# Kernel optimization log

Hardware: AMD Instinct MI355X
Metric: run time of the kernel (lower is better)

The kernel has to match this reference:

```python
import jax, jax.numpy as jnp
import numpy as np

B, T, NEMBD, HEAD = 8, 2048, 1024, 64

def setup_inputs() -> dict:
    key = jax.random.key(0)
    ks = jax.random.split(key, 6)
    return {
        "values": jax.random.normal(ks[0], (B, T, NEMBD), dtype=jnp.float32),
        "keys": jax.random.normal(ks[1], (B, T, NEMBD), dtype=jnp.float32),
        "queries": jax.random.normal(ks[2], (B, T, NEMBD), dtype=jnp.float32),
        "Wk": jax.random.normal(ks[3], (NEMBD, HEAD), dtype=jnp.float32) * (NEMBD ** -0.5),
        "Wq": jax.random.normal(ks[4], (NEMBD, HEAD), dtype=jnp.float32) * (NEMBD ** -0.5),
        "Wv": jax.random.normal(ks[5], (NEMBD, HEAD), dtype=jnp.float32) * (NEMBD ** -0.5),
    }

def reference(values, keys, queries, Wk, Wq, Wv):
    Bq, Tq, C = queries.shape  # C = nEmbd; original scales by C**-0.5 (NOT headSize)
    k = keys @ Wk              # [B,T,H]
    q = queries @ Wq           # [B,T,H]
    v = values @ Wv            # [B,T,H]
    weight = jnp.einsum('bth,bsh->bts', q, k) * (C ** -0.5)  # [B,T,T]
    causal = jnp.tril(jnp.ones((Tq, Tq), dtype=bool))
    weight = jnp.where(causal, weight, -jnp.inf)
    weight = jax.nn.softmax(weight, axis=-1)
    # dropout = 0.0 (eval): identity
    out = jnp.einsum('bts,bsh->bth', weight, v)  # [B,T,H]
    return out
```

## Files before the change

### kernel.cpp

```cpp
#include <hip/hip_runtime.h>
#include <hip/hip_bf16.h>

typedef __bf16 bf16x8 __attribute__((ext_vector_type(8)));
typedef float f32x4 __attribute__((ext_vector_type(4)));
typedef unsigned short u16x8 __attribute__((ext_vector_type(8)));

#define NB 8
#define NT 2048
#define NC 1024
#define NH 64

__device__ __forceinline__ unsigned short bfbits(float f) {
    return __builtin_bit_cast(unsigned short, (__bf16)f);
}

__global__ __launch_bounds__(256) void wt_kernel(const float* __restrict__ Wq,
                                                 const float* __restrict__ Wk,
                                                 const float* __restrict__ Wv,
                                                 unsigned short* __restrict__ Wt) {
    int idx = blockIdx.x * 256 + threadIdx.x;
    int n = idx >> 16;
    int r = idx & 65535;
    int c = r >> 6;
    int h = r & 63;
    const float* W = (n == 0) ? Wq : ((n == 1) ? Wk : Wv);
    float x = W[c * 64 + h];
    Wt[(n << 16) + h * 1024 + c] = bfbits(x);
}

__global__ __launch_bounds__(256, 4) void proj_kernel(const float* __restrict__ Xv,
                                                      const float* __restrict__ Xk,
                                                      const float* __restrict__ Xq,
                                                      const unsigned short* __restrict__ Wt,
                                                      unsigned short* __restrict__ Q,
                                                      unsigned short* __restrict__ K,
                                                      unsigned short* __restrict__ VT) {
    __shared__ __align__(16) char Xs[64 * 256];
    __shared__ __align__(16) char Ws[64 * 256];

    int type = blockIdx.x >> 8;
    int mt   = blockIdx.x & 255;
    int row0 = mt << 6;
    const float* X = (type == 0) ? Xq : ((type == 1) ? Xk : Xv);
    const unsigned short* W = Wt + (type << 16);

    int tid  = threadIdx.x;
    int w    = tid >> 6;
    int lane = tid & 63;
    int lo = lane & 15, hi = lane >> 4;

    f32x4 acc[4];
#pragma unroll
    for (int ct = 0; ct < 4; ++ct) acc[ct] = 0.f;

    for (int kc = 0; kc < 8; ++kc) {
        f32x4 xr[8];
#pragma unroll
        for (int i = 0; i < 8; ++i) {
            int f4 = tid + 256 * i;
            int r  = f4 >> 5, c4 = f4 & 31;
            xr[i] = __builtin_nontemporal_load(
                (const f32x4*)(X + (size_t)(row0 + r) * NC + kc * 128 + c4 * 4));
        }
        u16x8 wr_[4];
#pragma unroll
        for (int i = 0; i < 4; ++i) {
            int s16 = tid + 256 * i;
            int h = s16 >> 4, sl = s16 & 15;
            wr_[i] = *(const u16x8*)(W + h * 1024 + kc * 128 + sl * 8);
        }
        __syncthreads();
#pragma unroll
        for (int i = 0; i < 8; ++i) {
            int f4 = tid + 256 * i;
            int r  = f4 >> 5, c4 = f4 & 31;
            ushort4 bv;
            bv.x = bfbits(xr[i][0]); bv.y = bfbits(xr[i][1]);
            bv.z = bfbits(xr[i][2]); bv.w = bfbits(xr[i][3]);
            int byte = r * 256 + ((c4 * 8) ^ ((r & 7) << 4));
            *(ushort4*)(Xs + byte) = bv;
        }
#pragma unroll
        for (int i = 0; i < 4; ++i) {
            int s16 = tid + 256 * i;
            int h = s16 >> 4, sl = s16 & 15;
            int byte = h * 256 + ((sl * 16) ^ ((h & 7) << 4));
            *(u16x8*)(Ws + byte) = wr_[i];
        }
        __syncthreads();
#pragma unroll
        for (int ks = 0; ks < 4; ++ks) {
            int coff = (ks * 64 + hi * 16) ^ ((lo & 7) << 4);
            bf16x8 af = *(const bf16x8*)(Xs + (w * 16 + lo) * 256 + coff);
#pragma unroll
            for (int ct = 0; ct < 4; ++ct) {
                bf16x8 bf = *(const bf16x8*)(Ws + (ct * 16 + lo) * 256 + coff);
                acc[ct] = __builtin_amdgcn_mfma_f32_16x16x32_bf16(af, bf, acc[ct], 0, 0, 0);
            }
        }
    }

    if (type < 2) {
        unsigned short* O = (type == 0) ? Q : K;
#pragma unroll
        for (int ct = 0; ct < 4; ++ct)
#pragma unroll
            for (int r = 0; r < 4; ++r) {
                int row = row0 + w * 16 + hi * 4 + r;
                int h = lo + 16 * ct;
                O[(size_t)row * NH + h] = bfbits(acc[ct][r]);
            }
    } else {
        int trow = row0 + w * 16 + hi * 4;
        int b = trow >> 11;
        int t = trow & 2047;
#pragma unroll
        for (int ct = 0; ct < 4; ++ct) {
            int h = lo + 16 * ct;
            ushort4 pk;
            pk.x = bfbits(acc[ct][0]);
            pk.y = bfbits(acc[ct][1]);
            pk.z = bfbits(acc[ct][2]);
            pk.w = bfbits(acc[ct][3]);
            *(ushort4*)(VT + (size_t)(b * NH + h) * NT + t) = pk;
        }
    }
}

__global__ __launch_bounds__(256) void attn_kernel(const unsigned short* __restrict__ Q,
                                                   const unsigned short* __restrict__ K,
                                                   const unsigned short* __restrict__ VT,
                                                   float* __restrict__ out) {
    __shared__ __align__(16) unsigned short p_lds[4 * 1024];
    __shared__ __align__(16) float acc_lds[4 * 16 * 64];
    __shared__ float l_lds[4][16];

    int b  = blockIdx.x & 7;
    int qt = 127 - (blockIdx.x >> 3);
    int q0 = qt << 4;
    int w    = threadIdx.x >> 6;
    int lane = threadIdx.x & 63;
    int lo = lane & 15, hi = lane >> 4;

    const float SC = 0.03125f * 1.44269504088896340736f;
    const unsigned short* qb = Q + (size_t)(b * NT + q0 + lo) * NH + hi * 8;
    bf16x8 qr0 = *(const bf16x8*)(qb);
    bf16x8 qr1 = *(const bf16x8*)(qb + 32);
    bf16x8 qf0, qf1;
#pragma unroll
    for (int jj = 0; jj < 8; ++jj) {
        qf0[jj] = (__bf16)((float)qr0[jj] * SC);
        qf1[jj] = (__bf16)((float)qr1[jj] * SC);
    }

    int Ct = (q0 + 79) >> 6;
    int c0 = (Ct * w) >> 2;
    int c1 = (Ct * (w + 1)) >> 2;

    float l[4];
    f32x4 acc[4];
#pragma unroll
    for (int r = 0; r < 4; ++r) l[r] = 0.f;
#pragma unroll
    for (int ct = 0; ct < 4; ++ct) acc[ct] = 0.f;

    unsigned short* pl = p_lds + w * 1024;
    char* plb = (char*)pl;

    bf16x8 kn[8];
    {
        const unsigned short* kp = K + (size_t)(b * NT + (c0 << 6) + lo) * NH + hi * 8;
#pragma unroll
        for (int g = 0; g < 4; ++g) {
            kn[2 * g]     = *(const bf16x8*)(kp + g * 16 * NH);
            kn[2 * g + 1] = *(const bf16x8*)(kp + g * 16 * NH + 32);
        }
    }

    for (int c = c0; c < c1; ++c) {
        int s0 = c << 6;
        bf16x8 kk[8];
#pragma unroll
        for (int i = 0; i < 8; ++i) kk[i] = kn[i];
        const unsigned short* vb = VT + (size_t)(b * NH + lo) * NT + s0 + hi * 8;
        bf16x8 vA0 = *(const bf16x8*)(vb);
        bf16x8 vA1 = *(const bf16x8*)(vb + 16 * NT);
        bf16x8 vA2 = *(const bf16x8*)(vb + 32 * NT);
        bf16x8 vA3 = *(const bf16x8*)(vb + 48 * NT);
        bf16x8 vB0 = *(const bf16x8*)(vb + 32);
        bf16x8 vB1 = *(const bf16x8*)(vb + 16 * NT + 32);
        bf16x8 vB2 = *(const bf16x8*)(vb + 32 * NT + 32);
        bf16x8 vB3 = *(const bf16x8*)(vb + 48 * NT + 32);
        if (c + 1 < c1) {
            const unsigned short* kp2 = K + (size_t)(b * NT + ((c + 1) << 6) + lo) * NH + hi * 8;
#pragma unroll
            for (int g = 0; g < 4; ++g) {
                kn[2 * g]     = *(const bf16x8*)(kp2 + g * 16 * NH);
                kn[2 * g + 1] = *(const bf16x8*)(kp2 + g * 16 * NH + 32);
            }
        }

        f32x4 S[4];
#pragma unroll
        for (int t = 0; t < 4; ++t) {
            f32x4 s = 0.f;
            s = __builtin_amdgcn_mfma_f32_16x16x32_bf16(qf0, kk[2 * t], s, 0, 0, 0);
            s = __builtin_amdgcn_mfma_f32_16x16x32_bf16(qf1, kk[2 * t + 1], s, 0, 0, 0);
            S[t] = s;
        }

#pragma unroll
        for (int r = 0; r < 4; ++r) {
            int qi = q0 + hi * 4 + r;
            int ql = hi * 4 + r;
            int sw = (ql & 7) << 4;
            float psum = 0.f;
#pragma unroll
            for (int t = 0; t < 4; ++t) {
                int sk = s0 + t * 16 + lo;
                float p = (sk <= qi) ? exp2f(S[t][r] - 32.f) : 0.f;
                psum += p;
                int byte = ql * 128 + ((((t * 16 + lo) * 2)) ^ sw);
                *(unsigned short*)(plb + byte) = bfbits(p);
            }
            l[r] += psum;
        }

        int rsw = (lo & 7) << 4;
        bf16x8 pa0 = *(const bf16x8*)(plb + lo * 128 + ((hi * 16) ^ rsw));
        bf16x8 pa1 = *(const bf16x8*)(plb + lo * 128 + (((4 + hi) * 16) ^ rsw));
        acc[0] = __builtin_amdgcn_mfma_f32_16x16x32_bf16(pa0, vA0, acc[0], 0, 0, 0);
        acc[1] = __builtin_amdgcn_mfma_f32_16x16x32_bf16(pa0, vA1, acc[1], 0, 0, 0);
        acc[2] = __builtin_amdgcn_mfma_f32_16x16x32_bf16(pa0, vA2, acc[2], 0, 0, 0);
        acc[3] = __builtin_amdgcn_mfma_f32_16x16x32_bf16(pa0, vA3, acc[3], 0, 0, 0);
        acc[0] = __builtin_amdgcn_mfma_f32_16x16x32_bf16(pa1, vB0, acc[0], 0, 0, 0);
        acc[1] = __builtin_amdgcn_mfma_f32_16x16x32_bf16(pa1, vB1, acc[1], 0, 0, 0);
        acc[2] = __builtin_amdgcn_mfma_f32_16x16x32_bf16(pa1, vB2, acc[2], 0, 0, 0);
        acc[3] = __builtin_amdgcn_mfma_f32_16x16x32_bf16(pa1, vB3, acc[3], 0, 0, 0);
    }

#pragma unroll
    for (int d = 1; d < 16; d <<= 1)
#pragma unroll
        for (int r = 0; r < 4; ++r)
            l[r] += __shfl_xor(l[r], d, 16);

#pragma unroll
    for (int r = 0; r < 4; ++r) {
        int ql = hi * 4 + r;
#pragma unroll
        for (int ct = 0; ct < 4; ++ct)
            acc_lds[(w * 16 + ql) * 64 + lo + 16 * ct] = acc[ct][r];
    }
    if (lo == 0) {
#pragma unroll
        for (int r = 0; r < 4; ++r)
            l_lds[w][hi * 4 + r] = l[r];
    }
    __syncthreads();

    int q  = threadIdx.x >> 4;
    int h0 = (threadIdx.x & 15) << 2;
    float L = l_lds[0][q] + l_lds[1][q] + l_lds[2][q] + l_lds[3][q];
    float ox = 0.f, oy = 0.f, oz = 0.f, ow = 0.f;
#pragma unroll
    for (int ww = 0; ww < 4; ++ww) {
        const float* p = acc_lds + (ww * 16 + q) * 64 + h0;
        ox += p[0]; oy += p[1]; oz += p[2]; ow += p[3];
    }
    float inv = 1.0f / L;
    float4 res = make_float4(ox * inv, oy * inv, oz * inv, ow * inv);
    *(float4*)(out + (size_t)(b * NT + q0 + q) * NH + h0) = res;
}

extern "C" void kernel_launch(void* const* d_in, const int* in_sizes, int n_in,
                              void* d_out, int out_size, void* d_ws, size_t ws_size,
                              hipStream_t stream) {
    const float* values  = (const float*)d_in[0];
    const float* keys    = (const float*)d_in[1];
    const float* queries = (const float*)d_in[2];
    const float* Wk = (const float*)d_in[3];
    const float* Wq = (const float*)d_in[4];
    const float* Wv = (const float*)d_in[5];
    float* out = (float*)d_out;

    unsigned short* Wt = (unsigned short*)d_ws;
    unsigned short* Qb = Wt + 196608;
    unsigned short* Kb = Qb + 1048576;
    unsigned short* VT = Kb + 1048576;

    wt_kernel<<<768, 256, 0, stream>>>(Wq, Wk, Wv, Wt);
    proj_kernel<<<768, 256, 0, stream>>>(values, keys, queries, Wt, Qb, Kb, VT);
    attn_kernel<<<1024, 256, 0, stream>>>(Qb, Kb, VT, out);
}
```

Measured before the change: 83.94 us.

## Double-buffer projection GEMM with direct global-to-LDS async loads

The projection kernel now loads X tiles (as fp32) and weight tiles straight into LDS with global_load_lds, double-buffered over 16 smaller k-chunks, and converts X to bf16 on the LDS read side. A staggered start chunk per block spreads the access pattern, and explicit vmcnt waits plus barriers replace the register-staging __syncthreads pipeline. The aim is to overlap memory loads with MFMA work and cut register pressure. LDS use doubles, so occupancy drops (launch bounds lowered to 3), and conversion work moves into the inner loop.

Result: faster. 80.02 us (-4.7%).

```diff
diff --git a/kernel.cpp b/kernel.cpp
--- a/kernel.cpp
+++ b/kernel.cpp
@@ -12,6 +12,17 @@
 
 __device__ __forceinline__ unsigned short bfbits(float f) {
     return __builtin_bit_cast(unsigned short, (__bf16)f);
+}
+
+__device__ __forceinline__ void gl_lds16(const void* g, void* l) {
+    __builtin_amdgcn_global_load_lds(
+        (const __attribute__((address_space(1))) void*)g,
+        (__attribute__((address_space(3))) void*)l, 16, 0, 0);
+}
+__device__ __forceinline__ void gl_lds16_nt(const void* g, void* l) {
+    __builtin_amdgcn_global_load_lds(
+        (const __attribute__((address_space(1))) void*)g,
+        (__attribute__((address_space(3))) void*)l, 16, 0, 2);
 }
 
 __global__ __launch_bounds__(256) void wt_kernel(const float* __restrict__ Wq,
@@ -28,75 +39,87 @@
     Wt[(n << 16) + h * 1024 + c] = bfbits(x);
 }
 
-__global__ __launch_bounds__(256, 4) void proj_kernel(const float* __restrict__ Xv,
+__global__ __launch_bounds__(256, 3) void proj_kernel(const float* __restrict__ Xv,
                                                       const float* __restrict__ Xk,
                                                       const float* __restrict__ Xq,
                                                       const unsigned short* __restrict__ Wt,
                                                       unsigned short* __restrict__ Q,
                                                       unsigned short* __restrict__ K,
                                                       unsigned short* __restrict__ VT) {
-    __shared__ __align__(16) char Xs[64 * 256];
-    __shared__ __align__(16) char Ws[64 * 256];
+    __shared__ __align__(16) char Xs[2][16384];
+    __shared__ __align__(16) char Ws[2][8192];
 
     int type = blockIdx.x >> 8;
     int mt   = blockIdx.x & 255;
     int row0 = mt << 6;
+    int phase = mt & 15;
     const float* X = (type == 0) ? Xq : ((type == 1) ? Xk : Xv);
-    const unsigned short* W = Wt + (type << 16);
 
     int tid  = threadIdx.x;
     int w    = tid >> 6;
     int lane = tid & 63;
     int lo = lane & 15, hi = lane >> 4;
+    int swz = (lo & 7) << 4;
+
+    const char* Xbase = (const char*)X + (size_t)row0 * 4096;
+    const char* Wbase = (const char*)(Wt + (type << 16));
+
+    int xr_l = lane >> 4;
+    int xc_l = (lane & 15) * 16;
+    int wr_l = lane >> 3;
+    int wc_l = (lane & 7) * 16;
 
     f32x4 acc[4];
 #pragma unroll
     for (int ct = 0; ct < 4; ++ct) acc[ct] = 0.f;
 
-    for (int kc = 0; kc < 8; ++kc) {
-        f32x4 xr[8];
-#pragma unroll
-        for (int i = 0; i < 8; ++i) {
-            int f4 = tid + 256 * i;
-            int r  = f4 >> 5, c4 = f4 & 31;
-            xr[i] = __builtin_nontemporal_load(
-                (const f32x4*)(X + (size_t)(row0 + r) * NC + kc * 128 + c4 * 4));
-        }
-        u16x8 wr_[4];
+    auto stage = [&](int kc, int buf) {
 #pragma unroll
         for (int i = 0; i < 4; ++i) {
-            int s16 = tid + 256 * i;
-            int h = s16 >> 4, sl = s16 & 15;
-            wr_[i] = *(const u16x8*)(W + h * 1024 + kc * 128 + sl * 8);
-        }
-        __syncthreads();
-#pragma unroll
-        for (int i = 0; i < 8; ++i) {
-            int f4 = tid + 256 * i;
-            int r  = f4 >> 5, c4 = f4 & 31;
-            ushort4 bv;
-            bv.x = bfbits(xr[i][0]); bv.y = bfbits(xr[i][1]);
-            bv.z = bfbits(xr[i][2]); bv.w = bfbits(xr[i][3]);
-            int byte = r * 256 + ((c4 * 8) ^ ((r & 7) << 4));
-            *(ushort4*)(Xs + byte) = bv;
-        }
-#pragma unroll
-        for (int i = 0; i < 4; ++i) {
-            int s16 = tid + 256 * i;
-            int h = s16 >> 4, sl = s16 & 15;
-            int byte = h * 256 + ((sl * 16) ^ ((h & 7) << 4));
-            *(u16x8*)(Ws + byte) = wr_[i];
-        }
-        __syncthreads();
-#pragma unroll
-        for (int ks = 0; ks < 4; ++ks) {
-            int coff = (ks * 64 + hi * 16) ^ ((lo & 7) << 4);
-            bf16x8 af = *(const bf16x8*)(Xs + (w * 16 + lo) * 256 + coff);
+            int g = w * 4 + i;
+            int r = g * 4 + xr_l;
+            gl_lds16_nt(Xbase + (size_t)r * 4096 + kc * 256 + (xc_l ^ ((r & 7) << 4)),
+                        Xs[buf] + g * 1024);
+        }
+#pragma unroll
+        for (int i = 0; i < 2; ++i) {
+            int g = w * 2 + i;
+            int h = g * 8 + wr_l;
+            gl_lds16(Wbase + (size_t)h * 2048 + kc * 128 + (wc_l ^ ((h & 7) << 4)),
+                     Ws[buf] + g * 1024);
+        }
+    };
+
+    auto compute = [&](int buf) {
+        const char* xrow = Xs[buf] + (w * 16 + lo) * 256;
+        const char* wb   = Ws[buf];
+#pragma unroll
+        for (int ks = 0; ks < 2; ++ks) {
+            f32x4 a0 = *(const f32x4*)(xrow + ((ks * 128 + hi * 32) ^ swz));
+            f32x4 a1 = *(const f32x4*)(xrow + ((ks * 128 + hi * 32 + 16) ^ swz));
+            bf16x8 af;
+            af[0] = (__bf16)a0[0]; af[1] = (__bf16)a0[1]; af[2] = (__bf16)a0[2]; af[3] = (__bf16)a0[3];
+            af[4] = (__bf16)a1[0]; af[5] = (__bf16)a1[1]; af[6] = (__bf16)a1[2]; af[7] = (__bf16)a1[3];
 #pragma unroll
             for (int ct = 0; ct < 4; ++ct) {
-                bf16x8 bf = *(const bf16x8*)(Ws + (ct * 16 + lo) * 256 + coff);
+                bf16x8 bf = *(const bf16x8*)(wb + (ct * 16 + lo) * 128 + ((ks * 64 + hi * 16) ^ swz));
                 acc[ct] = __builtin_amdgcn_mfma_f32_16x16x32_bf16(af, bf, acc[ct], 0, 0, 0);
             }
+        }
+    };
+
+    stage(phase, 0);
+    stage((1 + phase) & 15, 1);
+
+    for (int c = 0; c < 16; ++c) {
+        int buf = c & 1;
+        if (c < 15) asm volatile("s_waitcnt vmcnt(6)" ::: "memory");
+        else        asm volatile("s_waitcnt vmcnt(0)" ::: "memory");
+        __builtin_amdgcn_s_barrier();
+        compute(buf);
+        if (c + 2 < 16) {
+            __builtin_amdgcn_s_barrier();
+            stage((c + 2 + phase) & 15, buf);
         }
     }
 
```
